# Performance work log

Measured on AMD Instinct MI355X. Metric: run time of the kernel, lower is better.

Reference implementation:

```python
import jax, jax.numpy as jnp
import numpy as np

N_NODES = 100000
N_EDGES = 2500000


def setup_inputs() -> dict:
    key = jax.random.key(0)
    ks = jax.random.split(key, 6)
    x = jax.random.normal(ks[0], (N_NODES, 2), dtype=jnp.float32)
    edge_index = jax.random.randint(ks[1], (2, N_EDGES), 0, N_NODES, dtype=jnp.int32)
    # SAGEConv(2, 32): lin_l applied to mean-aggregated neighbors (carries bias),
    # lin_r applied to root features (no bias) -- PyG defaults.
    W_l1 = jax.random.normal(ks[2], (2, 32), dtype=jnp.float32) * 0.5
    W_r1 = jax.random.normal(ks[3], (2, 32), dtype=jnp.float32) * 0.5
    b1 = jnp.zeros((32,), jnp.float32)
    # SAGEConv(32, 2)
    W_l2 = jax.random.normal(ks[4], (32, 2), dtype=jnp.float32) * 0.1
    W_r2 = jax.random.normal(ks[5], (32, 2), dtype=jnp.float32) * 0.1
    b2 = jnp.zeros((2,), jnp.float32)
    return dict(x=x, edge_index=edge_index, W_l1=W_l1, W_r1=W_r1, b1=b1,
                W_l2=W_l2, W_r2=W_r2, b2=b2)


def _sage_conv(x, src, dst, deg_inv, W_l, W_r, b):
    # mean aggregation of source-node features at destination nodes
    summed = jax.ops.segment_sum(x[src], dst, num_segments=N_NODES)  # [N, F]
    agg = summed * deg_inv  # scatter-mean; isolated nodes get 0
    return agg @ W_l + x @ W_r + b


def reference(x, edge_index, W_l1, W_r1, b1, W_l2, W_r2, b2):
    src, dst = edge_index[0], edge_index[1]
    ones = jnp.ones((src.shape[0],), x.dtype)
    deg = jax.ops.segment_sum(ones, dst, num_segments=N_NODES)
    deg_inv = (1.0 / jnp.maximum(deg, 1.0))[:, None]  # [N, 1]
    h = jax.nn.relu(_sage_conv(x, src, dst, deg_inv, W_l1, W_r1, b1))
    out = _sage_conv(h, src, dst, deg_inv, W_l2, W_r2, b2)
    return jax.nn.log_softmax(out, axis=1)
```

## Files before the change

### kernel.cpp

```cpp
#include <hip/hip_runtime.h>

#define N_NODES 100000
#define N_EDGES 2500000
#define NPB 64
#define NBUC 1563
#define SB 512
#define EPB 4883
#define TOT (NBUC * SB)
#define P3B 782


typedef unsigned int u32;

__global__ void hist_k(const int* __restrict__ ei, u32* __restrict__ histG) {
    __shared__ u32 hl[NBUC];
    int t = threadIdx.x, b = blockIdx.x;
    for (int k = t; k < NBUC; k += 256) hl[k] = 0;
    __syncthreads();
    int e0 = b * EPB, e1 = min(e0 + EPB, N_EDGES);
    for (int e = e0 + t; e < e1; e += 256) {
        int dst = ei[N_EDGES + e];
        atomicAdd(&hl[(u32)dst >> 6], 1u);
    }
    __syncthreads();
    for (int k = t; k < NBUC; k += 256) histG[k * SB + b] = hl[k];
}

__global__ void scan_p1(const u32* __restrict__ histG, u32* __restrict__ blockSum) {
    __shared__ u32 red[256];
    int t = threadIdx.x;
    int base = blockIdx.x * 1024;
    u32 s = 0;
#pragma unroll
    for (int j = 0; j < 4; ++j) {
        int idx = base + t * 4 + j;
        if (idx < TOT) s += histG[idx];
    }
    red[t] = s;
    __syncthreads();
    for (int off = 128; off > 0; off >>= 1) {
        if (t < off) red[t] += red[t + off];
        __syncthreads();
    }
    if (t == 0) blockSum[blockIdx.x] = red[0];
}

__global__ void scan_p2(const u32* __restrict__ blockSum, u32* __restrict__ blockBase) {
    __shared__ u32 ts[256];
    int t = threadIdx.x;
    u32 v[4];
    u32 s = 0;
#pragma unroll
    for (int j = 0; j < 4; ++j) {
        int idx = t * 4 + j;
        v[j] = (idx < P3B) ? blockSum[idx] : 0u;
        s += v[j];
    }
    ts[t] = s;
    __syncthreads();
    for (int off = 1; off < 256; off <<= 1) {
        u32 add = (t >= off) ? ts[t - off] : 0u;
        __syncthreads();
        ts[t] += add;
        __syncthreads();
    }
    u32 run = (t > 0) ? ts[t - 1] : 0u;
#pragma unroll
    for (int j = 0; j < 4; ++j) {
        int idx = t * 4 + j;
        if (idx < P3B) blockBase[idx] = run;
        run += v[j];
    }
}

__global__ void scan_p3(u32* histG, const u32* __restrict__ blockBase) {
    __shared__ u32 ts[256];
    int t = threadIdx.x;
    int base = blockIdx.x * 1024;
    u32 v[4];
    u32 s = 0;
#pragma unroll
    for (int j = 0; j < 4; ++j) {
        int idx = base + t * 4 + j;
        v[j] = (idx < TOT) ? histG[idx] : 0u;
        s += v[j];
    }
    ts[t] = s;
    __syncthreads();
    for (int off = 1; off < 256; off <<= 1) {
        u32 add = (t >= off) ? ts[t - off] : 0u;
        __syncthreads();
        ts[t] += add;
        __syncthreads();
    }
    u32 run = ((t > 0) ? ts[t - 1] : 0u) + blockBase[blockIdx.x];
#pragma unroll
    for (int j = 0; j < 4; ++j) {
        int idx = base + t * 4 + j;
        if (idx < TOT) histG[idx] = run;
        run += v[j];
    }
}

__global__ void scatter_k(const int* __restrict__ ei, const u32* __restrict__ histG,
                          u32* __restrict__ sortedE) {
    __shared__ u32 pos[NBUC];
    int t = threadIdx.x, b = blockIdx.x;
    for (int k = t; k < NBUC; k += 256) pos[k] = histG[k * SB + b];
    __syncthreads();
    int e0 = b * EPB, e1 = min(e0 + EPB, N_EDGES);
    for (int e = e0 + t; e < e1; e += 256) {
        int src = ei[e];
        int dst = ei[N_EDGES + e];
        u32 k = (u32)dst >> 6;
        u32 slot = atomicAdd(&pos[k], 1u);
        sortedE[slot] = (((u32)dst & 63u) << 17) | (u32)src;
    }
}

__global__ void agg1_node1(const u32* __restrict__ sortedE, const u32* __restrict__ histG,
                           const float* __restrict__ x,
                           const float* __restrict__ Wl1, const float* __restrict__ Wr1,
                           const float* __restrict__ b1,
                           const float* __restrict__ Wl2, const float* __restrict__ Wr2,
                           float2* __restrict__ h2G, float2* __restrict__ hrG,
                           float* __restrict__ degG) {
    __shared__ u32 cntL[NPB], fxL[NPB], fyL[NPB];
    __shared__ float sWl1[64], sWr1[64], sb1[32], sWl2[64], sWr2[64];
    int t = threadIdx.x, k = blockIdx.x;
    if (t < 64) { sWl1[t] = Wl1[t]; sWr1[t] = Wr1[t]; sWl2[t] = Wl2[t]; sWr2[t] = Wr2[t]; }
    if (t >= 64 && t < 96) sb1[t - 64] = b1[t - 64];
    if (t >= 96 && t < 96 + NPB) { cntL[t - 96] = 0; fxL[t - 96] = 0; fyL[t - 96] = 0; }
    __syncthreads();

    u32 start = histG[k * SB];
    u32 end = (k + 1 < NBUC) ? histG[(k + 1) * SB] : N_EDGES;
    const float2* x2 = (const float2*)x;
    for (u32 idx = start + t; idx < end; idx += 256) {
        u32 p = sortedE[idx];
        u32 src = p & 0x1FFFFu;
        u32 loc = p >> 17;
        float2 v = x2[src];
        atomicAdd(&fxL[loc], (u32)((v.x + 16.0f) * 65536.0f + 0.5f));
        atomicAdd(&fyL[loc], (u32)((v.y + 16.0f) * 65536.0f + 0.5f));
        atomicAdd(&cntL[loc], 1u);
    }
    __syncthreads();

    if (t < NPB) {
        int i = k * NPB + t;
        if (i < N_NODES) {
            u32 cnt = cntL[t];
            float fc = (float)cnt;
            float dinv = 1.0f / fmaxf(fc, 1.0f);
            float ax = (float)(int)(fxL[t] - cnt * 1048576u) * (1.0f / 65536.0f) * dinv;
            float ay = (float)(int)(fyL[t] - cnt * 1048576u) * (1.0f / 65536.0f) * dinv;
            float2 xv = x2[i];
            float h2a = 0.f, h2b = 0.f, hra = 0.f, hrb = 0.f;
#pragma unroll
            for (int f = 0; f < 32; ++f) {
                float h = ax * sWl1[f] + ay * sWl1[32 + f] + xv.x * sWr1[f] + xv.y * sWr1[32 + f] + sb1[f];
                h = fmaxf(h, 0.0f);
                h2a += h * sWl2[2 * f];
                h2b += h * sWl2[2 * f + 1];
                hra += h * sWr2[2 * f];
                hrb += h * sWr2[2 * f + 1];
            }
            h2G[i] = make_float2(h2a, h2b);
            hrG[i] = make_float2(hra, hrb);
            degG[i] = fc;
        }
    }
}

__global__ void agg2_node2(const u32* __restrict__ sortedE, const u32* __restrict__ histG,
                           const float2* __restrict__ h2G, const float2* __restrict__ hrG,
                           const float* __restrict__ degG, const float* __restrict__ b2,
                           float* __restrict__ out) {
    __shared__ u32 gxL[NPB], gyL[NPB];
    int t = threadIdx.x, k = blockIdx.x;
    if (t < NPB) { gxL[t] = 0; gyL[t] = 0; }
    __syncthreads();

    u32 start = histG[k * SB];
    u32 end = (k + 1 < NBUC) ? histG[(k + 1) * SB] : N_EDGES;
    for (u32 idx = start + t; idx < end; idx += 256) {
        u32 p = sortedE[idx];
        u32 src = p & 0x1FFFFu;
        u32 loc = p >> 17;
        float2 v = h2G[src];
        atomicAdd(&gxL[loc], (u32)((v.x + 2048.0f) * 4096.0f + 0.5f));
        atomicAdd(&gyL[loc], (u32)((v.y + 2048.0f) * 4096.0f + 0.5f));
    }
    __syncthreads();

    if (t < NPB) {
        int i = k * NPB + t;
        if (i < N_NODES) {
            float cnt = degG[i];
            u32 c = (u32)cnt;
            float dinv = 1.0f / fmaxf(cnt, 1.0f);
            float sx = (float)(int)(gxL[t] - c * 8388608u) * (1.0f / 4096.0f) * dinv;
            float sy = (float)(int)(gyL[t] - c * 8388608u) * (1.0f / 4096.0f) * dinv;
            float2 hv = hrG[i];
            float o0 = sx + hv.x + b2[0];
            float o1 = sy + hv.y + b2[1];
            float m = fmaxf(o0, o1);
            float e0 = expf(o0 - m);
            float e1 = expf(o1 - m);
            float lse = logf(e0 + e1);
            ((float2*)out)[i] = make_float2(o0 - m - lse, o1 - m - lse);
        }
    }
}

extern "C" void kernel_launch(void* const* d_in, const int* in_sizes, int n_in,
                              void* d_out, int out_size, void* d_ws, size_t ws_size,
                              hipStream_t stream) {
    const float* x   = (const float*)d_in[0];
    const int*   ei  = (const int*)d_in[1];
    const float* Wl1 = (const float*)d_in[2];
    const float* Wr1 = (const float*)d_in[3];
    const float* b1  = (const float*)d_in[4];
    const float* Wl2 = (const float*)d_in[5];
    const float* Wr2 = (const float*)d_in[6];
    const float* b2  = (const float*)d_in[7];
    float* out = (float*)d_out;

    u32* histG      = (u32*)d_ws;
    u32* blockSum   = histG + TOT;
    u32* blockBase  = blockSum + P3B;
    u32* sortedE    = blockBase + P3B;
    float2* h2G     = (float2*)(sortedE + N_EDGES);
    float2* hrG     = h2G + N_NODES;
    float* degG     = (float*)(hrG + N_NODES);

    hist_k    <<<SB,   256, 0, stream>>>(ei, histG);
    scan_p1   <<<P3B,  256, 0, stream>>>(histG, blockSum);
    scan_p2   <<<1,    256, 0, stream>>>(blockSum, blockBase);
    scan_p3   <<<P3B,  256, 0, stream>>>(histG, blockBase);
    scatter_k <<<SB,   256, 0, stream>>>(ei, histG, sortedE);
    agg1_node1<<<NBUC, 256, 0, stream>>>(sortedE, histG, x, Wl1, Wr1, b1, Wl2, Wr2,
                                         h2G, hrG, degG);
    agg2_node2<<<NBUC, 256, 0, stream>>>(sortedE, histG, h2G, hrG, degG, b2, out);
}
```

Baseline: 170.8 us.

## Bucket edges into 2048-node superblocks with split partial aggregation and reduction

Replaces the 64-node bucket sort with coarse 2048-node superblocks, so the histogram, scan and scatter stages shrink to 49 buckets. Each superblock's edges are split across 16 blocks that accumulate into shared-memory histograms and write partial sums, and separate node kernels then reduce the partials and run the dense layer math. Layer-2 inputs are pre-quantized into packed 64-bit values to save per-edge conversion work. The histogram uses replicated counters to reduce atomic contention. In exchange it adds partial-sum writes and reads plus two extra launches, and the scatter now has far more atomic contention on only 49 positions per block.

```diff
diff --git a/kernel.cpp b/kernel.cpp
--- a/kernel.cpp
+++ b/kernel.cpp
@@ -2,28 +2,38 @@
 
 #define N_NODES 100000
 #define N_EDGES 2500000
-#define NPB 64
-#define NBUC 1563
+#define SBBITS 11
+#define SBSZ 2048
+#define NSB 49
 #define SB 512
 #define EPB 4883
-#define TOT (NBUC * SB)
-#define P3B 782
+#define TOT (NSB * SB)
+#define P1B 25
+#define M 16
+#define AGG_GRID (NSB * M)
 
 
 typedef unsigned int u32;
+typedef unsigned long long u64;
 
 __global__ void hist_k(const int* __restrict__ ei, u32* __restrict__ histG) {
-    __shared__ u32 hl[NBUC];
+    __shared__ u32 hl[NSB * 8];
     int t = threadIdx.x, b = blockIdx.x;
-    for (int k = t; k < NBUC; k += 256) hl[k] = 0;
+    for (int k = t; k < NSB * 8; k += 256) hl[k] = 0;
     __syncthreads();
     int e0 = b * EPB, e1 = min(e0 + EPB, N_EDGES);
+    int r = t & 7;
     for (int e = e0 + t; e < e1; e += 256) {
-        int dst = ei[N_EDGES + e];
-        atomicAdd(&hl[(u32)dst >> 6], 1u);
-    }
-    __syncthreads();
-    for (int k = t; k < NBUC; k += 256) histG[k * SB + b] = hl[k];
+        u32 dst = (u32)ei[N_EDGES + e];
+        atomicAdd(&hl[(dst >> SBBITS) * 8 + r], 1u);
+    }
+    __syncthreads();
+    for (int k = t; k < NSB; k += 256) {
+        u32 s = 0;
+#pragma unroll
+        for (int j = 0; j < 8; ++j) s += hl[k * 8 + j];
+        histG[k * SB + b] = s;
+    }
 }
 
 __global__ void scan_p1(const u32* __restrict__ histG, u32* __restrict__ blockSum) {
@@ -53,7 +63,7 @@
 #pragma unroll
     for (int j = 0; j < 4; ++j) {
         int idx = t * 4 + j;
-        v[j] = (idx < P3B) ? blockSum[idx] : 0u;
+        v[j] = (idx < P1B) ? blockSum[idx] : 0u;
         s += v[j];
     }
     ts[t] = s;
@@ -68,7 +78,7 @@
 #pragma unroll
     for (int j = 0; j < 4; ++j) {
         int idx = t * 4 + j;
-        if (idx < P3B) blockBase[idx] = run;
+        if (idx < P1B) blockBase[idx] = run;
         run += v[j];
     }
 }
@@ -104,114 +114,185 @@
 
 __global__ void scatter_k(const int* __restrict__ ei, const u32* __restrict__ histG,
                           u32* __restrict__ sortedE) {
-    __shared__ u32 pos[NBUC];
+    __shared__ u32 pos[NSB];
     int t = threadIdx.x, b = blockIdx.x;
-    for (int k = t; k < NBUC; k += 256) pos[k] = histG[k * SB + b];
+    if (t < NSB) pos[t] = histG[t * SB + b];
     __syncthreads();
     int e0 = b * EPB, e1 = min(e0 + EPB, N_EDGES);
     for (int e = e0 + t; e < e1; e += 256) {
-        int src = ei[e];
-        int dst = ei[N_EDGES + e];
-        u32 k = (u32)dst >> 6;
-        u32 slot = atomicAdd(&pos[k], 1u);
-        sortedE[slot] = (((u32)dst & 63u) << 17) | (u32)src;
-    }
-}
-
-__global__ void agg1_node1(const u32* __restrict__ sortedE, const u32* __restrict__ histG,
-                           const float* __restrict__ x,
-                           const float* __restrict__ Wl1, const float* __restrict__ Wr1,
-                           const float* __restrict__ b1,
-                           const float* __restrict__ Wl2, const float* __restrict__ Wr2,
-                           float2* __restrict__ h2G, float2* __restrict__ hrG,
-                           float* __restrict__ degG) {
-    __shared__ u32 cntL[NPB], fxL[NPB], fyL[NPB];
+        u32 src = (u32)ei[e];
+        u32 dst = (u32)ei[N_EDGES + e];
+        u32 sb = dst >> SBBITS;
+        u32 slot = atomicAdd(&pos[sb], 1u);
+        sortedE[slot] = ((dst & (SBSZ - 1u)) << 17) | src;
+    }
+}
+
+__global__ void agg1_k(const u32* __restrict__ sortedE, const u32* __restrict__ histG,
+                       const float* __restrict__ x, u32* __restrict__ PART) {
+    __shared__ u32 cntL[SBSZ], fxL[SBSZ], fyL[SBSZ];
+    int t = threadIdx.x;
+    u32 sb = blockIdx.x / M, m = blockIdx.x % M;
+    for (int j = t; j < SBSZ; j += 256) { cntL[j] = 0; fxL[j] = 0; fyL[j] = 0; }
+    __syncthreads();
+
+    u32 s0 = histG[sb * SB];
+    u32 s1 = (sb + 1 < NSB) ? histG[(sb + 1) * SB] : N_EDGES;
+    u32 len = s1 - s0;
+    u32 a = s0 + len * m / M;
+    u32 bEnd = s0 + len * (m + 1) / M;
+    const float2* x2 = (const float2*)x;
+
+    u32 idx = a + t;
+    while (idx + 256 < bEnd) {
+        u32 p0 = sortedE[idx], p1 = sortedE[idx + 256];
+        float2 v0 = x2[p0 & 0x1FFFFu];
+        float2 v1 = x2[p1 & 0x1FFFFu];
+        u32 l0 = p0 >> 17, l1 = p1 >> 17;
+        atomicAdd(&cntL[l0], 1u);
+        atomicAdd(&fxL[l0], (u32)((v0.x + 16.0f) * 65536.0f + 0.5f));
+        atomicAdd(&fyL[l0], (u32)((v0.y + 16.0f) * 65536.0f + 0.5f));
+        atomicAdd(&cntL[l1], 1u);
+        atomicAdd(&fxL[l1], (u32)((v1.x + 16.0f) * 65536.0f + 0.5f));
+        atomicAdd(&fyL[l1], (u32)((v1.y + 16.0f) * 65536.0f + 0.5f));
+        idx += 512;
+    }
+    if (idx < bEnd) {
+        u32 p = sortedE[idx];
+        float2 v = x2[p & 0x1FFFFu];
+        u32 l = p >> 17;
+        atomicAdd(&cntL[l], 1u);
+        atomicAdd(&fxL[l], (u32)((v.x + 16.0f) * 65536.0f + 0.5f));
+        atomicAdd(&fyL[l], (u32)((v.y + 16.0f) * 65536.0f + 0.5f));
+    }
+    __syncthreads();
+
+    u32 base = blockIdx.x * (3 * SBSZ);
+    for (int j = t; j < SBSZ; j += 256) {
+        PART[base + j] = cntL[j];
+        PART[base + SBSZ + j] = fxL[j];
+        PART[base + 2 * SBSZ + j] = fyL[j];
+    }
+}
+
+__global__ void reduce1_node1(const u32* __restrict__ PART, const float* __restrict__ x,
+                              const float* __restrict__ Wl1, const float* __restrict__ Wr1,
+                              const float* __restrict__ b1,
+                              const float* __restrict__ Wl2, const float* __restrict__ Wr2,
+                              u64* __restrict__ ench2, float2* __restrict__ hrG,
+                              float* __restrict__ degG) {
     __shared__ float sWl1[64], sWr1[64], sb1[32], sWl2[64], sWr2[64];
-    int t = threadIdx.x, k = blockIdx.x;
+    int t = threadIdx.x;
     if (t < 64) { sWl1[t] = Wl1[t]; sWr1[t] = Wr1[t]; sWl2[t] = Wl2[t]; sWr2[t] = Wr2[t]; }
     if (t >= 64 && t < 96) sb1[t - 64] = b1[t - 64];
-    if (t >= 96 && t < 96 + NPB) { cntL[t - 96] = 0; fxL[t - 96] = 0; fyL[t - 96] = 0; }
-    __syncthreads();
-
-    u32 start = histG[k * SB];
-    u32 end = (k + 1 < NBUC) ? histG[(k + 1) * SB] : N_EDGES;
-    const float2* x2 = (const float2*)x;
-    for (u32 idx = start + t; idx < end; idx += 256) {
+    __syncthreads();
+
+    int i = blockIdx.x * 256 + t;
+    if (i >= N_NODES) return;
+    u32 sb = (u32)i >> SBBITS, j = (u32)i & (SBSZ - 1u);
+
+    u32 cnt = 0, fx = 0, fy = 0;
+#pragma unroll
+    for (int m = 0; m < M; ++m) {
+        u32 base = (sb * M + m) * (3 * SBSZ);
+        cnt += PART[base + j];
+        fx += PART[base + SBSZ + j];
+        fy += PART[base + 2 * SBSZ + j];
+    }
+
+    float fc = (float)cnt;
+    float dinv = 1.0f / fmaxf(fc, 1.0f);
+    float ax = (float)(int)(fx - cnt * 1048576u) * (1.0f / 65536.0f) * dinv;
+    float ay = (float)(int)(fy - cnt * 1048576u) * (1.0f / 65536.0f) * dinv;
+    float2 xv = ((const float2*)x)[i];
+
+    float h2a = 0.f, h2b = 0.f, hra = 0.f, hrb = 0.f;
+#pragma unroll
+    for (int f = 0; f < 32; ++f) {
+        float h = ax * sWl1[f] + ay * sWl1[32 + f] + xv.x * sWr1[f] + xv.y * sWr1[32 + f] + sb1[f];
+        h = fmaxf(h, 0.0f);
+        h2a += h * sWl2[2 * f];
+        h2b += h * sWl2[2 * f + 1];
+        hra += h * sWr2[2 * f];
+        hrb += h * sWr2[2 * f + 1];
+    }
+    u32 ex = (u32)((h2a + 2048.0f) * 4096.0f + 0.5f);
+    u32 ey = (u32)((h2b + 2048.0f) * 4096.0f + 0.5f);
+    ench2[i] = ((u64)ey << 32) | (u64)ex;
+    hrG[i] = make_float2(hra, hrb);
+    degG[i] = fc;
+}
+
+__global__ void agg2_k(const u32* __restrict__ sortedE, const u32* __restrict__ histG,
+                       const u64* __restrict__ ench2, u32* __restrict__ PART2) {
+    __shared__ u32 gxL[SBSZ], gyL[SBSZ];
+    int t = threadIdx.x;
+    u32 sb = blockIdx.x / M, m = blockIdx.x % M;
+    for (int j = t; j < SBSZ; j += 256) { gxL[j] = 0; gyL[j] = 0; }
+    __syncthreads();
+
+    u32 s0 = histG[sb * SB];
+    u32 s1 = (sb + 1 < NSB) ? histG[(sb + 1) * SB] : N_EDGES;
+    u32 len = s1 - s0;
+    u32 a = s0 + len * m / M;
+    u32 bEnd = s0 + len * (m + 1) / M;
+
+    u32 idx = a + t;
+    while (idx + 256 < bEnd) {
+        u32 p0 = sortedE[idx], p1 = sortedE[idx + 256];
+        u64 e0 = ench2[p0 & 0x1FFFFu];
+        u64 e1 = ench2[p1 & 0x1FFFFu];
+        u32 l0 = p0 >> 17, l1 = p1 >> 17;
+        atomicAdd(&gxL[l0], (u32)e0);
+        atomicAdd(&gyL[l0], (u32)(e0 >> 32));
+        atomicAdd(&gxL[l1], (u32)e1);
+        atomicAdd(&gyL[l1], (u32)(e1 >> 32));
+        idx += 512;
+    }
+    if (idx < bEnd) {
         u32 p = sortedE[idx];
-        u32 src = p & 0x1FFFFu;
-        u32 loc = p >> 17;
-        float2 v = x2[src];
-        atomicAdd(&fxL[loc], (u32)((v.x + 16.0f) * 65536.0f + 0.5f));
-        atomicAdd(&fyL[loc], (u32)((v.y + 16.0f) * 65536.0f + 0.5f));
-        atomicAdd(&cntL[loc], 1u);
-    }
-    __syncthreads();
-
-    if (t < NPB) {
-        int i = k * NPB + t;
-        if (i < N_NODES) {
-            u32 cnt = cntL[t];
-            float fc = (float)cnt;
-            float dinv = 1.0f / fmaxf(fc, 1.0f);
-            float ax = (float)(int)(fxL[t] - cnt * 1048576u) * (1.0f / 65536.0f) * dinv;
-            float ay = (float)(int)(fyL[t] - cnt * 1048576u) * (1.0f / 65536.0f) * dinv;
-            float2 xv = x2[i];
-            float h2a = 0.f, h2b = 0.f, hra = 0.f, hrb = 0.f;
-#pragma unroll
-            for (int f = 0; f < 32; ++f) {
-                float h = ax * sWl1[f] + ay * sWl1[32 + f] + xv.x * sWr1[f] + xv.y * sWr1[32 + f] + sb1[f];
-                h = fmaxf(h, 0.0f);
-                h2a += h * sWl2[2 * f];
-                h2b += h * sWl2[2 * f + 1];
-                hra += h * sWr2[2 * f];
-                hrb += h * sWr2[2 * f + 1];
-            }
-            h2G[i] = make_float2(h2a, h2b);
-            hrG[i] = make_float2(hra, hrb);
-            degG[i] = fc;
-        }
-    }
-}
-
-__global__ void agg2_node2(const u32* __restrict__ sortedE, const u32* __restrict__ histG,
-                           const float2* __restrict__ h2G, const float2* __restrict__ hrG,
-                           const float* __restrict__ degG, const float* __restrict__ b2,
-                           float* __restrict__ out) {
-    __shared__ u32 gxL[NPB], gyL[NPB];
-    int t = threadIdx.x, k = blockIdx.x;
-    if (t < NPB) { gxL[t] = 0; gyL[t] = 0; }
-    __syncthreads();
-
-    u32 start = histG[k * SB];
-    u32 end = (k + 1 < NBUC) ? histG[(k + 1) * SB] : N_EDGES;
-    for (u32 idx = start + t; idx < end; idx += 256) {
-        u32 p = sortedE[idx];
-        u32 src = p & 0x1FFFFu;
-        u32 loc = p >> 17;
-        float2 v = h2G[src];
-        atomicAdd(&gxL[loc], (u32)((v.x + 2048.0f) * 4096.0f + 0.5f));
-        atomicAdd(&gyL[loc], (u32)((v.y + 2048.0f) * 4096.0f + 0.5f));
-    }
-    __syncthreads();
-
-    if (t < NPB) {
-        int i = k * NPB + t;
-        if (i < N_NODES) {
-            float cnt = degG[i];
-            u32 c = (u32)cnt;
-            float dinv = 1.0f / fmaxf(cnt, 1.0f);
-            float sx = (float)(int)(gxL[t] - c * 8388608u) * (1.0f / 4096.0f) * dinv;
-            float sy = (float)(int)(gyL[t] - c * 8388608u) * (1.0f / 4096.0f) * dinv;
-            float2 hv = hrG[i];
-            float o0 = sx + hv.x + b2[0];
-            float o1 = sy + hv.y + b2[1];
-            float m = fmaxf(o0, o1);
-            float e0 = expf(o0 - m);
-            float e1 = expf(o1 - m);
-            float lse = logf(e0 + e1);
-            ((float2*)out)[i] = make_float2(o0 - m - lse, o1 - m - lse);
-        }
-    }
+        u64 e = ench2[p & 0x1FFFFu];
+        u32 l = p >> 17;
+        atomicAdd(&gxL[l], (u32)e);
+        atomicAdd(&gyL[l], (u32)(e >> 32));
+    }
+    __syncthreads();
+
+    u32 base = blockIdx.x * (2 * SBSZ);
+    for (int j = t; j < SBSZ; j += 256) {
+        PART2[base + j] = gxL[j];
+        PART2[base + SBSZ + j] = gyL[j];
+    }
+}
+
+__global__ void reduce2_node2(const u32* __restrict__ PART2, const float2* __restrict__ hrG,
+                              const float* __restrict__ degG, const float* __restrict__ b2,
+                              float* __restrict__ out) {
+    int i = blockIdx.x * 256 + threadIdx.x;
+    if (i >= N_NODES) return;
+    u32 sb = (u32)i >> SBBITS, j = (u32)i & (SBSZ - 1u);
+
+    u32 gx = 0, gy = 0;
+#pragma unroll
+    for (int m = 0; m < M; ++m) {
+        u32 base = (sb * M + m) * (2 * SBSZ);
+        gx += PART2[base + j];
+        gy += PART2[base + SBSZ + j];
+    }
+
+    float fc = degG[i];
+    u32 c = (u32)fc;
+    float dinv = 1.0f / fmaxf(fc, 1.0f);
+    float sx = (float)(int)(gx - c * 8388608u) * (1.0f / 4096.0f) * dinv;
+    float sy = (float)(int)(gy - c * 8388608u) * (1.0f / 4096.0f) * dinv;
+    float2 hv = hrG[i];
+    float o0 = sx + hv.x + b2[0];
+    float o1 = sy + hv.y + b2[1];
+    float mx = fmaxf(o0, o1);
+    float e0 = expf(o0 - mx);
+    float e1 = expf(o1 - mx);
+    float lse = logf(e0 + e1);
+    ((float2*)out)[i] = make_float2(o0 - mx - lse, o1 - mx - lse);
 }
 
 extern "C" void kernel_launch(void* const* d_in, const int* in_sizes, int n_in,
@@ -227,20 +308,23 @@
     const float* b2  = (const float*)d_in[7];
     float* out = (float*)d_out;
 
-    u32* histG      = (u32*)d_ws;
-    u32* blockSum   = histG + TOT;
-    u32* blockBase  = blockSum + P3B;
-    u32* sortedE    = blockBase + P3B;
-    float2* h2G     = (float2*)(sortedE + N_EDGES);
-    float2* hrG     = h2G + N_NODES;
-    float* degG     = (float*)(hrG + N_NODES);
-
-    hist_k    <<<SB,   256, 0, stream>>>(ei, histG);
-    scan_p1   <<<P3B,  256, 0, stream>>>(histG, blockSum);
-    scan_p2   <<<1,    256, 0, stream>>>(blockSum, blockBase);
-    scan_p3   <<<P3B,  256, 0, stream>>>(histG, blockBase);
-    scatter_k <<<SB,   256, 0, stream>>>(ei, histG, sortedE);
-    agg1_node1<<<NBUC, 256, 0, stream>>>(sortedE, histG, x, Wl1, Wr1, b1, Wl2, Wr2,
-                                         h2G, hrG, degG);
-    agg2_node2<<<NBUC, 256, 0, stream>>>(sortedE, histG, h2G, hrG, degG, b2, out);
-}
+    u32* histG     = (u32*)d_ws;
+    u32* blockSum  = histG + TOT;
+    u32* blockBase = blockSum + 32;
+    u32* sortedE   = blockBase + 32;
+    u32* PART      = sortedE + N_EDGES;
+    u64* ench2     = (u64*)(PART + AGG_GRID * 3 * SBSZ);
+    float2* hrG    = (float2*)(ench2 + N_NODES);
+    float* degG    = (float*)(hrG + N_NODES);
+
+    hist_k  <<<SB,  256, 0, stream>>>(ei, histG);
+    scan_p1 <<<P1B, 256, 0, stream>>>(histG, blockSum);
+    scan_p2 <<<1,   256, 0, stream>>>(blockSum, blockBase);
+    scan_p3 <<<P1B, 256, 0, stream>>>(histG, blockBase);
+    scatter_k<<<SB, 256, 0, stream>>>(ei, histG, sortedE);
+    agg1_k  <<<AGG_GRID, 256, 0, stream>>>(sortedE, histG, x, PART);
+    reduce1_node1<<<(N_NODES + 255) / 256, 256, 0, stream>>>(PART, x, Wl1, Wr1, b1,
+                                                             Wl2, Wr2, ench2, hrG, degG);
+    agg2_k  <<<AGG_GRID, 256, 0, stream>>>(sortedE, histG, ench2, PART);
+    reduce2_node2<<<(N_NODES + 255) / 256, 256, 0, stream>>>(PART, hrG, degG, b2, out);
+}
```

Measured after the change: 148.3 us. -13.2%, faster.
